# Kernel tuning notes

Hardware: AMD Instinct MI355X
Metric: run time of the kernel (lower is better)

Reference implementation:

```python
import jax, jax.numpy as jnp
import numpy as np

B, H, V, L = 1024, 2048, 8192, 8


def setup_inputs() -> dict:
    key = jax.random.key(0)
    k1, k2, k3, k4 = jax.random.split(key, 4)
    state = jax.random.normal(k1, (B, H), dtype=jnp.float32)
    token = jax.random.randint(k2, (B,), 0, V, dtype=jnp.int64)
    ih = jax.random.normal(k3, (L, V, H), dtype=jnp.float32) * 0.02
    hh = jax.random.normal(k4, (L, H, H), dtype=jnp.float32) * 0.02
    return {"state": state, "token": token, "ih": ih, "hh": hh}


def reference(state, token, ih, hh):
    # Per layer: state = tanh(state + (state @ hh[i]) * ih[i][token])
    # ih[i][token]: gather -> [B, H]; state @ hh[i]: [B,H]@[H,H] -> [B,H]
    def step(s, layer_params):
        hh_i, ih_i = layer_params
        gate = ih_i[token]                      # [B, H] embedding gather
        s = jnp.tanh(s + (s @ hh_i) * gate)     # fused mul-add-tanh
        return s, None

    state, _ = jax.lax.scan(step, state, (hh, ih))
    return state
```

## Files before the change

### kernel.cpp

```cpp
#include <hip/hip_runtime.h>
#include <hip/hip_bf16.h>

#define B_DIM 1024
#define H_DIM 2048
#define V_DIM 8192
#define L_DIM 8

typedef __attribute__((ext_vector_type(8))) __bf16 bf16x8;
typedef __attribute__((ext_vector_type(4))) __bf16 bf16x4;
typedef __attribute__((ext_vector_type(4))) float f32x4;
typedef unsigned short u16;

#define ASM_BARRIER() asm volatile("s_barrier" ::: "memory")
#define WAIT_VM4() asm volatile("s_waitcnt vmcnt(4)" ::: "memory")
#define WAIT_VM0() asm volatile("s_waitcnt vmcnt(0)" ::: "memory")

__device__ __forceinline__ void async_copy16(const void* g, void* l) {
  __builtin_amdgcn_global_load_lds(
      (const unsigned int __attribute__((address_space(1)))*)g,
      (unsigned int __attribute__((address_space(3)))*)l,
      16, 0, 0);
}

__global__ __launch_bounds__(256) void rnn_conv_state(
    const float4* __restrict__ in, bf16x4* __restrict__ out) {
  int i = blockIdx.x * 256 + threadIdx.x;
  float4 v = in[i];
  bf16x4 o;
  o.x = (__bf16)v.x; o.y = (__bf16)v.y; o.z = (__bf16)v.z; o.w = (__bf16)v.w;
  out[i] = o;
}

__global__ __launch_bounds__(256) void rnn_hh_transpose_all(
    const float* __restrict__ hh, __bf16* __restrict__ hhT) {
  int bid = blockIdx.x;
  int l = bid >> 10;
  int t = bid & 1023;
  int k0 = (t >> 5) << 6;
  int n0 = (t & 31) << 6;
  __shared__ __bf16 tile[64][67];
  int tid = threadIdx.x;
  const float* hh_l = hh + ((size_t)l << 22);
  __bf16* hhT_l = hhT + ((size_t)l << 22);
  {
    int r = tid >> 2;
    int c = (tid & 3) << 4;
    const float4* src = (const float4*)(hh_l + (size_t)(k0 + r) * H_DIM + n0 + c);
#pragma unroll
    for (int q = 0; q < 4; q++) {
      float4 v = src[q];
      tile[r][c + q * 4 + 0] = (__bf16)v.x;
      tile[r][c + q * 4 + 1] = (__bf16)v.y;
      tile[r][c + q * 4 + 2] = (__bf16)v.z;
      tile[r][c + q * 4 + 3] = (__bf16)v.w;
    }
  }
  __syncthreads();
  {
    int n = tid >> 2;
    int kq = (tid & 3) << 4;
    alignas(16) u16 tmp[16];
#pragma unroll
    for (int j = 0; j < 16; j++) {
      __bf16 b = tile[kq + j][n];
      tmp[j] = *(const u16*)&b;
    }
    uint4* dst = (uint4*)(hhT_l + (size_t)(n0 + n) * H_DIM + k0 + kq);
    dst[0] = *(uint4*)(tmp);
    dst[1] = *(uint4*)(tmp + 8);
  }
}

__global__ __launch_bounds__(256) void rnn_layer_pipe(
    const __bf16* __restrict__ A, const __bf16* __restrict__ Bt,
    const float* __restrict__ S, const float* __restrict__ ih_l,
    const int* __restrict__ token,
    float* __restrict__ OutF, __bf16* __restrict__ OutB) {
  constexpr int K = H_DIM;
  constexpr int NT = K / 64;
  __shared__ __align__(16) __bf16 As[2][64 * 64];
  __shared__ __align__(16) __bf16 Bs[2][64 * 64];

  int bid = blockIdx.x;
  int x = bid & 7;
  int rest = bid >> 3;
  int mi = rest & 15;
  int ni = (rest >> 4) * 8 + x;
  int bm0 = mi * 64;
  int bn0 = ni * 64;

  int tid = threadIdx.x;
  int w = tid >> 6;
  int lane = tid & 63;
  int rsub = lane >> 3;
  int csw = (lane & 7) ^ rsub;

  const __bf16* pA0 = A + (size_t)(bm0 + (w * 2 + 0) * 8 + rsub) * K + csw * 8;
  const __bf16* pA1 = A + (size_t)(bm0 + (w * 2 + 1) * 8 + rsub) * K + csw * 8;
  const __bf16* pB0 = Bt + (size_t)(bn0 + (w * 2 + 0) * 8 + rsub) * K + csw * 8;
  const __bf16* pB1 = Bt + (size_t)(bn0 + (w * 2 + 1) * 8 + rsub) * K + csw * 8;
  int slot0 = (w * 2 + 0) * 512;
  int slot1 = (w * 2 + 1) * 512;

  int wm = (w >> 1) * 32;
  int wn = (w & 1) * 32;
  int col = lane & 15;
  int quad = lane >> 4;
  int c7 = lane & 7;

  f32x4 acc[2][2] = {};

  auto issue = [&](int buf, int kt) {
    int ko = kt * 64;
    async_copy16(pA0 + ko, &As[buf][slot0]);
    async_copy16(pA1 + ko, &As[buf][slot1]);
    async_copy16(pB0 + ko, &Bs[buf][slot0]);
    async_copy16(pB1 + ko, &Bs[buf][slot1]);
  };
  auto compute = [&](int buf) {
#pragma unroll
    for (int ks = 0; ks < 2; ks++) {
      int cc = ks * 4 + quad;
      bf16x8 a0 = *(const bf16x8*)(&As[buf][(wm + 0 + col) * 64 + ((cc ^ c7) * 8)]);
      bf16x8 a1 = *(const bf16x8*)(&As[buf][(wm + 16 + col) * 64 + ((cc ^ c7) * 8)]);
      bf16x8 b0 = *(const bf16x8*)(&Bs[buf][(wn + 0 + col) * 64 + ((cc ^ c7) * 8)]);
      bf16x8 b1 = *(const bf16x8*)(&Bs[buf][(wn + 16 + col) * 64 + ((cc ^ c7) * 8)]);
      acc[0][0] = __builtin_amdgcn_mfma_f32_16x16x32_bf16(a0, b0, acc[0][0], 0, 0, 0);
      acc[0][1] = __builtin_amdgcn_mfma_f32_16x16x32_bf16(a0, b1, acc[0][1], 0, 0, 0);
      acc[1][0] = __builtin_amdgcn_mfma_f32_16x16x32_bf16(a1, b0, acc[1][0], 0, 0, 0);
      acc[1][1] = __builtin_amdgcn_mfma_f32_16x16x32_bf16(a1, b1, acc[1][1], 0, 0, 0);
    }
  };

  issue(0, 0);
  for (int kt = 0; kt < NT; kt += 2) {
    issue(1, kt + 1);
    WAIT_VM4();
    ASM_BARRIER();
    compute(0);
    ASM_BARRIER();
    if (kt + 2 < NT) {
      issue(0, kt + 2);
      WAIT_VM4();
    } else {
      WAIT_VM0();
    }
    ASM_BARRIER();
    compute(1);
    ASM_BARRIER();
  }

#pragma unroll
  for (int mt = 0; mt < 2; mt++) {
#pragma unroll
    for (int reg = 0; reg < 4; reg++) {
      int b = bm0 + wm + mt * 16 + quad * 4 + reg;
      int tok = token[b];
      const float* ihrow = ih_l + (size_t)tok * H_DIM;
      size_t rowoff = (size_t)b * H_DIM;
#pragma unroll
      for (int nt = 0; nt < 2; nt++) {
        int h = bn0 + wn + nt * 16 + col;
        float g = ihrow[h];
        float sv = S[rowoff + h];
        float v = tanhf(fmaf(acc[mt][nt][reg], g, sv));
        OutF[rowoff + h] = v;
        OutB[rowoff + h] = (__bf16)v;
      }
    }
  }
}

extern "C" void kernel_launch(void* const* d_in, const int* in_sizes, int n_in,
                              void* d_out, int out_size, void* d_ws, size_t ws_size,
                              hipStream_t stream) {
  const float* state = (const float*)d_in[0];
  const int* token = (const int*)d_in[1];
  const float* ih = (const float*)d_in[2];
  const float* hh = (const float*)d_in[3];

  char* ws = (char*)d_ws;
  __bf16* hhT = (__bf16*)ws;
  float* F0 = (float*)(ws + 67108864);
  float* F1 = (float*)(ws + 75497472);
  __bf16* Sb0 = (__bf16*)(ws + 83886080);
  __bf16* Sb1 = (__bf16*)(ws + 88080384);

  rnn_hh_transpose_all<<<8192, 256, 0, stream>>>(hh, hhT);
  rnn_conv_state<<<2048, 256, 0, stream>>>((const float4*)state, (bf16x4*)Sb0);

  const float* Sprev = state;
  for (int l = 0; l < L_DIM; l++) {
    const __bf16* hhT_l = hhT + ((size_t)l << 22);
    const float* ih_l = ih + ((size_t)l << 24);
    const __bf16* Acur = (l & 1) ? Sb1 : Sb0;
    __bf16* outB = (l & 1) ? Sb0 : Sb1;
    float* outF = (l == L_DIM - 1) ? (float*)d_out : ((l & 1) ? F1 : F0);
    rnn_layer_pipe<<<512, 256, 0, stream>>>(Acur, hhT_l, Sprev, ih_l, token, outF, outB);
    Sprev = outF;
  }
}
```

Before: 924.3 us.

## Load GEMM fragments directly from global into registers, merge prep kernels

The layer GEMM no longer stages A and B tiles through LDS with async copies and barriers. Each wave now loads its MFMA operand fragments straight from global memory into a register double buffer. The two preprocessing kernels (weight transpose and state conversion) are merged into one launch. This removes LDS traffic, barriers and one launch, but each wave now reads operands that the other waves in the block share. That raises L2/global traffic, and the loads are strided 16-byte row accesses with no cross-wave reuse.

```diff
diff --git a/kernel.cpp b/kernel.cpp
--- a/kernel.cpp
+++ b/kernel.cpp
@@ -11,29 +11,20 @@
 typedef __attribute__((ext_vector_type(4))) float f32x4;
 typedef unsigned short u16;
 
-#define ASM_BARRIER() asm volatile("s_barrier" ::: "memory")
-#define WAIT_VM4() asm volatile("s_waitcnt vmcnt(4)" ::: "memory")
-#define WAIT_VM0() asm volatile("s_waitcnt vmcnt(0)" ::: "memory")
+#define MFMA16(a, b, c) __builtin_amdgcn_mfma_f32_16x16x32_bf16((a), (b), (c), 0, 0, 0)
 
-__device__ __forceinline__ void async_copy16(const void* g, void* l) {
-  __builtin_amdgcn_global_load_lds(
-      (const unsigned int __attribute__((address_space(1)))*)g,
-      (unsigned int __attribute__((address_space(3)))*)l,
-      16, 0, 0);
-}
-
-__global__ __launch_bounds__(256) void rnn_conv_state(
-    const float4* __restrict__ in, bf16x4* __restrict__ out) {
-  int i = blockIdx.x * 256 + threadIdx.x;
-  float4 v = in[i];
-  bf16x4 o;
-  o.x = (__bf16)v.x; o.y = (__bf16)v.y; o.z = (__bf16)v.z; o.w = (__bf16)v.w;
-  out[i] = o;
-}
-
-__global__ __launch_bounds__(256) void rnn_hh_transpose_all(
-    const float* __restrict__ hh, __bf16* __restrict__ hhT) {
+__global__ __launch_bounds__(256) void rnn_prep(
+    const float* __restrict__ hh, __bf16* __restrict__ hhT,
+    const float4* __restrict__ state, bf16x4* __restrict__ stateB) {
   int bid = blockIdx.x;
+  if (bid >= 8192) {
+    int i = (bid - 8192) * 256 + threadIdx.x;
+    float4 v = state[i];
+    bf16x4 o;
+    o.x = (__bf16)v.x; o.y = (__bf16)v.y; o.z = (__bf16)v.z; o.w = (__bf16)v.w;
+    stateB[i] = o;
+    return;
+  }
   int l = bid >> 10;
   int t = bid & 1023;
   int k0 = (t >> 5) << 6;
@@ -71,15 +62,13 @@
   }
 }
 
-__global__ __launch_bounds__(256) void rnn_layer_pipe(
+__global__ __launch_bounds__(256) void rnn_layer_direct(
     const __bf16* __restrict__ A, const __bf16* __restrict__ Bt,
     const float* __restrict__ S, const float* __restrict__ ih_l,
     const int* __restrict__ token,
     float* __restrict__ OutF, __bf16* __restrict__ OutB) {
   constexpr int K = H_DIM;
   constexpr int NT = K / 64;
-  __shared__ __align__(16) __bf16 As[2][64 * 64];
-  __shared__ __align__(16) __bf16 Bs[2][64 * 64];
 
   int bid = blockIdx.x;
   int x = bid & 7;
@@ -92,62 +81,47 @@
   int tid = threadIdx.x;
   int w = tid >> 6;
   int lane = tid & 63;
-  int rsub = lane >> 3;
-  int csw = (lane & 7) ^ rsub;
-
-  const __bf16* pA0 = A + (size_t)(bm0 + (w * 2 + 0) * 8 + rsub) * K + csw * 8;
-  const __bf16* pA1 = A + (size_t)(bm0 + (w * 2 + 1) * 8 + rsub) * K + csw * 8;
-  const __bf16* pB0 = Bt + (size_t)(bn0 + (w * 2 + 0) * 8 + rsub) * K + csw * 8;
-  const __bf16* pB1 = Bt + (size_t)(bn0 + (w * 2 + 1) * 8 + rsub) * K + csw * 8;
-  int slot0 = (w * 2 + 0) * 512;
-  int slot1 = (w * 2 + 1) * 512;
-
   int wm = (w >> 1) * 32;
   int wn = (w & 1) * 32;
   int col = lane & 15;
   int quad = lane >> 4;
-  int c7 = lane & 7;
+
+  const __bf16* pa0 = A + (size_t)(bm0 + wm + col) * K + quad * 8;
+  const __bf16* pa1 = pa0 + (size_t)16 * K;
+  const __bf16* pb0 = Bt + (size_t)(bn0 + wn + col) * K + quad * 8;
+  const __bf16* pb1 = pb0 + (size_t)16 * K;
 
   f32x4 acc[2][2] = {};
+  bf16x8 fa[2][2][2];
+  bf16x8 fb[2][2][2];
 
-  auto issue = [&](int buf, int kt) {
-    int ko = kt * 64;
-    async_copy16(pA0 + ko, &As[buf][slot0]);
-    async_copy16(pA1 + ko, &As[buf][slot1]);
-    async_copy16(pB0 + ko, &Bs[buf][slot0]);
-    async_copy16(pB1 + ko, &Bs[buf][slot1]);
-  };
-  auto compute = [&](int buf) {
+  auto loadT = [&](int buf, int kt) {
+    int o0 = kt * 64;
 #pragma unroll
     for (int ks = 0; ks < 2; ks++) {
-      int cc = ks * 4 + quad;
-      bf16x8 a0 = *(const bf16x8*)(&As[buf][(wm + 0 + col) * 64 + ((cc ^ c7) * 8)]);
-      bf16x8 a1 = *(const bf16x8*)(&As[buf][(wm + 16 + col) * 64 + ((cc ^ c7) * 8)]);
-      bf16x8 b0 = *(const bf16x8*)(&Bs[buf][(wn + 0 + col) * 64 + ((cc ^ c7) * 8)]);
-      bf16x8 b1 = *(const bf16x8*)(&Bs[buf][(wn + 16 + col) * 64 + ((cc ^ c7) * 8)]);
-      acc[0][0] = __builtin_amdgcn_mfma_f32_16x16x32_bf16(a0, b0, acc[0][0], 0, 0, 0);
-      acc[0][1] = __builtin_amdgcn_mfma_f32_16x16x32_bf16(a0, b1, acc[0][1], 0, 0, 0);
-      acc[1][0] = __builtin_amdgcn_mfma_f32_16x16x32_bf16(a1, b0, acc[1][0], 0, 0, 0);
-      acc[1][1] = __builtin_amdgcn_mfma_f32_16x16x32_bf16(a1, b1, acc[1][1], 0, 0, 0);
+      int o = o0 + ks * 32;
+      fa[buf][ks][0] = *(const bf16x8*)(pa0 + o);
+      fa[buf][ks][1] = *(const bf16x8*)(pa1 + o);
+      fb[buf][ks][0] = *(const bf16x8*)(pb0 + o);
+      fb[buf][ks][1] = *(const bf16x8*)(pb1 + o);
+    }
+  };
+  auto comp = [&](int buf) {
+#pragma unroll
+    for (int ks = 0; ks < 2; ks++) {
+      acc[0][0] = MFMA16(fa[buf][ks][0], fb[buf][ks][0], acc[0][0]);
+      acc[0][1] = MFMA16(fa[buf][ks][0], fb[buf][ks][1], acc[0][1]);
+      acc[1][0] = MFMA16(fa[buf][ks][1], fb[buf][ks][0], acc[1][0]);
+      acc[1][1] = MFMA16(fa[buf][ks][1], fb[buf][ks][1], acc[1][1]);
     }
   };
 
-  issue(0, 0);
+  loadT(0, 0);
   for (int kt = 0; kt < NT; kt += 2) {
-    issue(1, kt + 1);
-    WAIT_VM4();
-    ASM_BARRIER();
-    compute(0);
-    ASM_BARRIER();
-    if (kt + 2 < NT) {
-      issue(0, kt + 2);
-      WAIT_VM4();
-    } else {
-      WAIT_VM0();
-    }
-    ASM_BARRIER();
-    compute(1);
-    ASM_BARRIER();
+    loadT(1, kt + 1);
+    comp(0);
+    if (kt + 2 < NT) loadT(0, kt + 2);
+    comp(1);
   }
 
 #pragma unroll
@@ -186,8 +160,7 @@
   __bf16* Sb0 = (__bf16*)(ws + 83886080);
   __bf16* Sb1 = (__bf16*)(ws + 88080384);
 
-  rnn_hh_transpose_all<<<8192, 256, 0, stream>>>(hh, hhT);
-  rnn_conv_state<<<2048, 256, 0, stream>>>((const float4*)state, (bf16x4*)Sb0);
+  rnn_prep<<<10240, 256, 0, stream>>>(hh, hhT, (const float4*)state, (bf16x4*)Sb0);
 
   const float* Sprev = state;
   for (int l = 0; l < L_DIM; l++) {
@@ -196,7 +169,7 @@
     const __bf16* Acur = (l & 1) ? Sb1 : Sb0;
     __bf16* outB = (l & 1) ? Sb0 : Sb1;
     float* outF = (l == L_DIM - 1) ? (float*)d_out : ((l & 1) ? F1 : F0);
-    rnn_layer_pipe<<<512, 256, 0, stream>>>(Acur, hhT_l, Sprev, ih_l, token, outF, outB);
+    rnn_layer_direct<<<512, 256, 0, stream>>>(Acur, hhT_l, Sprev, ih_l, token, outF, outB);
     Sprev = outF;
   }
 }
```

After: 1.219 ms. +31.9%, slower.
